# Kernel optimization log

Hardware: AMD Instinct MI355X
Metric: run time of the kernel (lower is better)

Reference implementation:

```python
import jax, jax.numpy as jnp
import numpy as np

NUM_SONGS = 2000
N1 = NUM_SONGS + 1  # incl. padding idx 0
EMB = 64
B = 32
S = 5    # num_prev_shows
M = 25   # max_songs_per_show


def setup_inputs() -> dict:
    key = jax.random.key(0)
    ks = jax.random.split(key, 32)
    def lin(k, i, o):
        kw, kb = jax.random.split(k)
        s = 1.0 / np.sqrt(i)
        return (jax.random.uniform(kw, (i, o), jnp.float32, -s, s),
                jax.random.uniform(kb, (o,), jnp.float32, -s, s))
    song_emb = jax.random.normal(ks[0], (N1, EMB), jnp.float32)
    song_emb = song_emb.at[0].set(0.0)  # padding_idx=0
    gcn_w1, gcn_b1 = lin(ks[1], EMB, EMB)
    gcn_w2, gcn_b2 = lin(ks[2], EMB, EMB)
    q_w, q_b = lin(ks[3], EMB, EMB)
    k_w, k_b = lin(ks[4], EMB, EMB)
    v_w, v_b = lin(ks[5], EMB, EMB)
    venue_t = jax.random.normal(ks[6], (200, EMB // 4), jnp.float32)
    tour_t = jax.random.normal(ks[7], (20, EMB // 4), jnp.float32)
    country_t = jax.random.normal(ks[8], (50, EMB // 8), jnp.float32)
    fest_t = jax.random.normal(ks[9], (2, EMB // 8), jnp.float32)
    mara_t = jax.random.normal(ks[10], (2, EMB // 8), jnp.float32)
    ctx_in = EMB // 2 + 3 * (EMB // 8)  # 56
    ctx_w, ctx_b = lin(ks[11], ctx_in, EMB)
    p1_w, p1_b = lin(ks[12], EMB * 3, EMB * 2)
    p2_w, p2_b = lin(ks[13], EMB * 2, EMB)
    p3_w, p3_b = lin(ks[14], EMB, 1)
    return {
        'song_ids': jax.random.randint(ks[20], (B,), 0, N1),
        'prev_setlists': jax.random.randint(ks[21], (B, S, M), 0, N1),
        'venue_ids': jax.random.randint(ks[22], (B,), 0, 200),
        'tour_ids': jax.random.randint(ks[23], (B,), 0, 20),
        'country_ids': jax.random.randint(ks[24], (B,), 0, 50),
        'is_festival': jax.random.randint(ks[25], (B,), 0, 2),
        'is_marathon': jax.random.randint(ks[26], (B,), 0, 2),
        'song_emb': song_emb,
        'gcn_w1': gcn_w1, 'gcn_b1': gcn_b1, 'gcn_w2': gcn_w2, 'gcn_b2': gcn_b2,
        'q_w': q_w, 'q_b': q_b, 'k_w': k_w, 'k_b': k_b, 'v_w': v_w, 'v_b': v_b,
        'venue_t': venue_t, 'tour_t': tour_t, 'country_t': country_t,
        'fest_t': fest_t, 'mara_t': mara_t,
        'ctx_w': ctx_w, 'ctx_b': ctx_b,
        'p1_w': p1_w, 'p1_b': p1_b, 'p2_w': p2_w, 'p2_b': p2_b,
        'p3_w': p3_w, 'p3_b': p3_b,
    }


def _build_adj(prev_setlists):
    # co-occurrence counts via one scatter-add (replaces nested python loops)
    b, s, m = prev_setlists.shape
    mask = prev_setlists > 0
    pair_ok = (mask[:, :, :, None] & mask[:, :, None, :]
               & ~jnp.eye(m, dtype=bool))  # exclude same position i==j
    flat_idx = (prev_setlists[:, :, :, None] * N1
                + prev_setlists[:, :, None, :]).reshape(b, -1)
    w = pair_ok.astype(jnp.float32).reshape(b, -1)
    adj = jnp.zeros((b, N1 * N1), jnp.float32)
    adj = adj.at[jnp.arange(b)[:, None], flat_idx].add(w)
    adj = adj.reshape(b, N1, N1)
    return adj / (adj.sum(axis=2, keepdims=True) + 1e-10)


def _forward(song_ids, prev_setlists, venue_ids, tour_ids, country_ids,
             is_festival, is_marathon, song_emb, gcn_w1, gcn_b1, gcn_w2,
             gcn_b2, q_w, q_b, k_w, k_b, v_w, v_b, venue_t, tour_t,
             country_t, fest_t, mara_t, ctx_w, ctx_b, p1_w, p1_b, p2_w,
             p2_b, p3_w, p3_b):
    b = song_ids.shape[0]
    adj = _build_adj(prev_setlists)                      # [B,N1,N1]
    x = jnp.broadcast_to(song_emb[None], (b, N1, EMB))   # [B,N1,E]
    for w_, b_ in ((gcn_w1, gcn_b1), (gcn_w2, gcn_b2)):
        agg = jnp.einsum('bnm,bme->bne', adj, x)
        x = jax.nn.relu(agg @ w_ + b_)
    song_embs = x
    # ragged masked-mean show embeddings
    mask = (prev_setlists > 0).astype(jnp.float32)       # [B,S,M]
    gathered = jax.vmap(lambda se, ids: se[ids])(song_embs, prev_setlists)  # [B,S,M,E]
    cnt = mask.sum(-1, keepdims=True)                    # [B,S,1]
    show_embs = jnp.where(cnt > 0,
                          (gathered * mask[..., None]).sum(2) / jnp.maximum(cnt, 1.0),
                          0.0)                           # [B,S,E]
    ctx = jnp.concatenate([venue_t[venue_ids], tour_t[tour_ids],
                           country_t[country_ids], fest_t[is_festival],
                           mara_t[is_marathon]], axis=-1)
    ctx = ctx @ ctx_w + ctx_b                            # [B,E]
    # temporal attention
    q = ctx @ q_w + q_b                                  # [B,E]
    k = show_embs @ k_w + k_b                            # [B,S,E]
    v = show_embs @ v_w + v_b
    scores = jnp.einsum('be,bse->bs', q, k) / jnp.sqrt(jnp.float32(EMB))
    attn = jax.nn.softmax(scores, axis=-1)
    attended = jnp.einsum('bs,bse->be', attn, v)
    cand = song_embs[jnp.arange(b), song_ids]
    h = jnp.concatenate([cand, ctx, attended], axis=-1)  # [B,3E]
    h = jax.nn.relu(h @ p1_w + p1_b)   # dropout is eval-mode identity
    h = jax.nn.relu(h @ p2_w + p2_b)
    logits = (h @ p3_w + p3_b).squeeze(-1)
    return jax.nn.sigmoid(logits)


def reference(song_ids, prev_setlists, venue_ids, tour_ids, country_ids,
              is_festival, is_marathon, song_emb, gcn_w1, gcn_b1, gcn_w2,
              gcn_b2, q_w, q_b, k_w, k_b, v_w, v_b, venue_t, tour_t,
              country_t, fest_t, mara_t, ctx_w, ctx_b, p1_w, p1_b, p2_w,
              p2_b, p3_w, p3_b):
    return _forward(song_ids, prev_setlists, venue_ids, tour_ids,
                    country_ids, is_festival, is_marathon, song_emb,
                    gcn_w1, gcn_b1, gcn_w2, gcn_b2, q_w, q_b, k_w, k_b,
                    v_w, v_b, venue_t, tour_t, country_t, fest_t, mara_t,
                    ctx_w, ctx_b, p1_w, p1_b, p2_w, p2_b, p3_w, p3_b)
```

## Files before the change

kernel.cpp:

```cpp
#include <hip/hip_runtime.h>
#include <hip/hip_bf16.h>

#define N1    2001
#define EMB   64
#define NSHOW 5
#define MSONG 25
#define NPOS  (NSHOW * MSONG)
#define MAXU  128
#define NT    1024

__global__ __launch_bounds__(NT, 4)
void setsgnn_kernel(
    const int* __restrict__ song_ids,
    const int* __restrict__ prev_setlists,
    const int* __restrict__ venue_ids,
    const int* __restrict__ tour_ids,
    const int* __restrict__ country_ids,
    const int* __restrict__ is_festival,
    const int* __restrict__ is_marathon,
    const float* __restrict__ song_emb,
    const float* __restrict__ gcn_w1, const float* __restrict__ gcn_b1,
    const float* __restrict__ gcn_w2, const float* __restrict__ gcn_b2,
    const float* __restrict__ q_w,  const float* __restrict__ q_b,
    const float* __restrict__ k_w,  const float* __restrict__ k_b,
    const float* __restrict__ v_w,  const float* __restrict__ v_b,
    const float* __restrict__ venue_t, const float* __restrict__ tour_t,
    const float* __restrict__ country_t, const float* __restrict__ fest_t,
    const float* __restrict__ mara_t,
    const float* __restrict__ ctx_w, const float* __restrict__ ctx_b,
    const float* __restrict__ p1_w,  const float* __restrict__ p1_b,
    const float* __restrict__ p2_w,  const float* __restrict__ p2_b,
    const float* __restrict__ p3_w,  const float* __restrict__ p3_b,
    float* __restrict__ out)
{
    const int b    = blockIdx.x;
    const int tid  = threadIdx.x;
    const int wv   = tid >> 6;
    const int lane = tid & 63;

    __shared__ __align__(16) float xb0[MAXU][EMB];
    __shared__ __align__(16) float xb1[MAXU][EMB];
    __shared__ __align__(16) float wlds[2][EMB][EMB];
    __shared__ __align__(16) float blds[2][EMB];
    __shared__ __align__(16) float bias_ctx[EMB], bias_q[EMB], bias_k[EMB], bias_v[EMB];
    __shared__ __align__(16) float bias_p1[128], bias_p2[EMB], bias_p3w[EMB];
    __shared__ float bias_p3b;
    __shared__ unsigned short idmap[N1];
    __shared__ int   sl[NPOS];
    __shared__ int   pmap[NPOS];
    __shared__ int   list_ids[MAXU];
    __shared__ float c_us[MAXU][NSHOW];
    __shared__ float occv[MAXU];
    __shared__ float invv[MAXU];
    __shared__ float cntm1[NSHOW];
    __shared__ int   cnt_show[NSHOW];
    __shared__ int   U_cnt;
    __shared__ float Xsum[NSHOW][EMB];
    __shared__ float XW[NSHOW][EMB];
    __shared__ float show_e[NSHOW][EMB];
    __shared__ float ctxin[56];
    __shared__ float ctxv[EMB];
    __shared__ float qv[EMB];
    __shared__ float kvatt[NSHOW][EMB];
    __shared__ float vatt[NSHOW][EMB];
    __shared__ float attnw[NSHOW];
    __shared__ float hbuf[3 * EMB];
    __shared__ float h1b[128];
    __shared__ float h2b[EMB];
    __shared__ float partial[1024];

    const float4 g0 = ((const float4*)gcn_w1)[tid];
    const float4 g1 = ((const float4*)gcn_w2)[tid];
    float4 bb;
    if (tid < 32) bb = (tid < 16) ? ((const float4*)gcn_b1)[tid]
                                  : ((const float4*)gcn_b2)[tid - 16];
    const int sid    = song_ids[b];
    const int vid    = venue_ids[b];
    const int tourid = tour_ids[b];
    const int cid    = country_ids[b];
    const int fid    = is_festival[b];
    const int mid    = is_marathon[b];

    for (int i = tid; i < N1; i += NT) idmap[i] = 0xFFFFu;
    if (tid < NPOS) sl[tid] = prev_setlists[b * NPOS + tid];
    if (tid == 0) U_cnt = 0;
    ((float4*)wlds)[tid]      = g0;
    ((float4*)wlds)[NT + tid] = g1;
    if (tid < 32) ((float4*)blds)[tid] = bb;
    {
        int r = tid - 256;
        if (r >= 0 && r < 16)        ((float4*)bias_ctx)[r]       = ((const float4*)ctx_b)[r];
        else if (r >= 16 && r < 32)  ((float4*)bias_q)[r - 16]    = ((const float4*)q_b)[r - 16];
        else if (r >= 32 && r < 48)  ((float4*)bias_k)[r - 32]    = ((const float4*)k_b)[r - 32];
        else if (r >= 48 && r < 64)  ((float4*)bias_v)[r - 48]    = ((const float4*)v_b)[r - 48];
        else if (r >= 64 && r < 96)  ((float4*)bias_p1)[r - 64]   = ((const float4*)p1_b)[r - 64];
        else if (r >= 96 && r < 112) ((float4*)bias_p2)[r - 96]   = ((const float4*)p2_b)[r - 96];
        else if (r >= 112 && r < 128)((float4*)bias_p3w)[r - 112] = ((const float4*)p3_w)[r - 112];
        else if (r == 128)           bias_p3b = p3_b[0];
    }
    __syncthreads();

    if (tid < NPOS) { int id = sl[tid]; if (id > 0) idmap[id] = 1u; }
    if (tid == 0) idmap[sid] = 1u;
    __syncthreads();

    for (int i = tid; i < N1; i += NT) {
        if (idmap[i] == 1u) {
            int u = atomicAdd(&U_cnt, 1);
            idmap[i] = (unsigned short)u;
            list_ids[u] = i;
        }
    }
    __syncthreads();
    const int U = U_cnt;

    if (tid < NPOS) { int id = sl[tid]; pmap[tid] = (id > 0) ? (int)idmap[id] : -1; }
    for (int t = tid; t < MAXU * NSHOW; t += NT) ((float*)c_us)[t] = 0.f;
    if (tid < NSHOW) {
        int c = 0;
        for (int i = 0; i < MSONG; i++) c += (sl[tid * MSONG + i] > 0) ? 1 : 0;
        cnt_show[tid] = c; cntm1[tid] = (float)(c - 1);
    }
    __syncthreads();

    if (tid < NPOS) { int pm = pmap[tid]; if (pm >= 0) atomicAdd(&c_us[pm][tid / MSONG], 1.f); }
    for (int t = tid; t < MAXU * (EMB / 4); t += NT) {
        int u = t >> 4, e4 = t & 15;
        float4 v = make_float4(0.f, 0.f, 0.f, 0.f);
        if (u < U) v = ((const float4*)(song_emb + list_ids[u] * EMB))[e4];
        *(float4*)&xb0[u][e4 * 4] = v;
    }
    __syncthreads();

    if (tid < MAXU) {
        float o = 0.f, r = 0.f;
        #pragma unroll
        for (int s = 0; s < NSHOW; s++) { float cc = c_us[tid][s]; o += cc; r += cc * cntm1[s]; }
        occv[tid] = o; invv[tid] = 1.f / (r + 1e-10f);
    }
    {
        int e = tid - MAXU;
        if (e >= 0 && e < 56) {
            float val;
            if (e < 16)      val = venue_t[vid * 16 + e];
            else if (e < 32) val = tour_t[tourid * 16 + (e - 16)];
            else if (e < 40) val = country_t[cid * 8 + (e - 32)];
            else if (e < 48) val = fest_t[fid * 8 + (e - 40)];
            else             val = mara_t[mid * 8 + (e - 48)];
            ctxin[e] = val;
        }
    }
    __syncthreads();

    if (tid < EMB) {
        float acc = bias_ctx[tid];
        #pragma unroll
        for (int e = 0; e < 56; e++) acc += ctxin[e] * ctx_w[e * EMB + tid];
        ctxv[tid] = acc;
    }
    __syncthreads();

    if (tid < EMB) {
        float acc = bias_q[tid];
        #pragma unroll
        for (int e = 0; e < EMB; e++) acc += ctxv[e] * q_w[e * EMB + tid];
        qv[tid] = acc;
    }
    if (tid >= EMB && tid < EMB + NSHOW * EMB) {
        int t = tid - EMB, s = t >> 6, e = t & 63;
        float acc = 0.f;
        #pragma unroll
        for (int i = 0; i < MSONG; i++) { int pm = pmap[s * MSONG + i]; if (pm >= 0) acc += xb0[pm][e]; }
        Xsum[s][e] = acc;
    }
    __syncthreads();

    {
        float wcol[EMB];
        for (int l = 0; l < 2; ++l) {
            float (*xc)[EMB] = l ? xb1 : xb0;
            float (*xn)[EMB] = l ? xb0 : xb1;

            #pragma unroll
            for (int e = 0; e < EMB; e++) wcol[e] = wlds[l][e][lane];
            if (tid < NSHOW * EMB) {
                int s = tid >> 6, col = tid & 63;
                float acc = 0.f;
                #pragma unroll
                for (int e = 0; e < EMB; e++) acc += Xsum[s][e] * wlds[l][e][col];
                XW[s][col] = acc;
            }
            const float bias = blds[l][lane];
            __syncthreads();

            float4 kreg, vreg;
            if (l == 1) { kreg = ((const float4*)k_w)[tid]; vreg = ((const float4*)v_w)[tid]; }

            for (int u = wv; u < U; u += 16) {
                float a0 = 0.f, a1 = 0.f, a2 = 0.f, a3 = 0.f;
                #pragma unroll
                for (int e4 = 0; e4 < 16; e4++) {
                    const float4 a = *(const float4*)&xc[u][e4 * 4];
                    a0 += a.x * wcol[e4 * 4];
                    a1 += a.y * wcol[e4 * 4 + 1];
                    a2 += a.z * wcol[e4 * 4 + 2];
                    a3 += a.w * wcol[e4 * 4 + 3];
                }
                float y   = (a0 + a1) + (a2 + a3);
                float acc = c_us[u][0] * XW[0][lane] + c_us[u][1] * XW[1][lane]
                          + c_us[u][2] * XW[2][lane] + c_us[u][3] * XW[3][lane]
                          + c_us[u][4] * XW[4][lane];
                float val = (acc - occv[u] * y) * invv[u] + bias;
                xn[u][lane] = fmaxf(val, 0.f);
            }
            if (l == 1) { ((float4*)wlds)[tid] = kreg; ((float4*)wlds)[NT + tid] = vreg; }
            __syncthreads();

            if (l == 0) {
                if (tid < NSHOW * EMB) {
                    int s = tid >> 6, e = tid & 63;
                    float acc = 0.f;
                    #pragma unroll
                    for (int i = 0; i < MSONG; i++) { int pm = pmap[s * MSONG + i]; if (pm >= 0) acc += xb1[pm][e]; }
                    Xsum[s][e] = acc;
                }
                __syncthreads();
            }
        }
    }

    const int kk1 = tid >> 7, o1 = tid & 127;
    const int kk2 = tid >> 6, o2 = lane;
    float p1wr[24], p2wr[8];
    #pragma unroll
    for (int j = 0; j < 24; j++) p1wr[j] = p1_w[(kk1 * 24 + j) * 128 + o1];
    #pragma unroll
    for (int j = 0; j < 8; j++)  p2wr[j] = p2_w[(kk2 * 8 + j) * 64 + o2];

    if (tid < NSHOW * EMB) {
        int s = tid >> 6, e = tid & 63;
        float acc = 0.f;
        #pragma unroll
        for (int i = 0; i < MSONG; i++) { int pm = pmap[s * MSONG + i]; if (pm >= 0) acc += xb0[pm][e]; }
        int cs = cnt_show[s];
        show_e[s][e] = (cs > 0) ? acc / (float)cs : 0.f;
    }
    __syncthreads();

    if (tid < 2 * NSHOW * EMB) {
        int m = (tid >= NSHOW * EMB) ? 1 : 0;
        int t = m ? tid - NSHOW * EMB : tid;
        int s = t >> 6, col = t & 63;
        float acc = m ? bias_v[col] : bias_k[col];
        #pragma unroll
        for (int e = 0; e < EMB; e++) acc += show_e[s][e] * wlds[m][e][col];
        if (m) vatt[s][col] = acc; else kvatt[s][col] = acc;
    }
    __syncthreads();

    if (wv < NSHOW) {
        float p = qv[lane] * kvatt[wv][lane];
        #pragma unroll
        for (int o = 32; o > 0; o >>= 1) p += __shfl_xor(p, o, 64);
        if (lane == 0) attnw[wv] = p * 0.125f;
    }
    __syncthreads();
    if (tid == 0) {
        float mx = attnw[0];
        for (int s = 1; s < NSHOW; s++) mx = fmaxf(mx, attnw[s]);
        float sum = 0.f;
        for (int s = 0; s < NSHOW; s++) { float ev = expf(attnw[s] - mx); attnw[s] = ev; sum += ev; }
        float isum = 1.f / sum;
        for (int s = 0; s < NSHOW; s++) attnw[s] *= isum;
    }
    __syncthreads();

    if (tid < EMB) {
        float acc = 0.f;
        #pragma unroll
        for (int s = 0; s < NSHOW; s++) acc += attnw[s] * vatt[s][tid];
        hbuf[2 * EMB + tid] = acc;
        hbuf[EMB + tid]     = ctxv[tid];
        hbuf[tid]           = xb0[(int)idmap[sid]][tid];
    }
    __syncthreads();

    {
        float acc = (kk1 == 0) ? bias_p1[o1] : 0.f;
        #pragma unroll
        for (int j = 0; j < 24; j++) acc += hbuf[kk1 * 24 + j] * p1wr[j];
        partial[kk1 * 128 + o1] = acc;
    }
    __syncthreads();
    if (tid < 128) {
        float acc = 0.f;
        #pragma unroll
        for (int kk = 0; kk < 8; kk++) acc += partial[kk * 128 + tid];
        h1b[tid] = fmaxf(acc, 0.f);
    }
    __syncthreads();

    {
        float acc = (kk2 == 0) ? bias_p2[o2] : 0.f;
        #pragma unroll
        for (int j = 0; j < 8; j++) acc += h1b[kk2 * 8 + j] * p2wr[j];
        partial[kk2 * 64 + o2] = acc;
    }
    __syncthreads();
    if (tid < 64) {
        float acc = 0.f;
        #pragma unroll
        for (int kk = 0; kk < 16; kk++) acc += partial[kk * 64 + tid];
        h2b[tid] = fmaxf(acc, 0.f);
    }
    __syncthreads();

    if (wv == 0) {
        float p = h2b[lane] * bias_p3w[lane];
        #pragma unroll
        for (int o = 32; o > 0; o >>= 1) p += __shfl_xor(p, o, 64);
        if (lane == 0) out[b] = 1.f / (1.f + expf(-(p + bias_p3b)));
    }
}

extern "C" void kernel_launch(void* const* d_in, const int* in_sizes, int n_in,
                              void* d_out, int out_size, void* d_ws, size_t ws_size,
                              hipStream_t stream) {
    (void)n_in; (void)out_size; (void)d_ws; (void)ws_size;
    const int B = in_sizes[0];
    setsgnn_kernel<<<B, NT, 0, stream>>>(
        (const int*)d_in[0], (const int*)d_in[1], (const int*)d_in[2],
        (const int*)d_in[3], (const int*)d_in[4], (const int*)d_in[5],
        (const int*)d_in[6],
        (const float*)d_in[7],
        (const float*)d_in[8],  (const float*)d_in[9],
        (const float*)d_in[10], (const float*)d_in[11],
        (const float*)d_in[12], (const float*)d_in[13],
        (const float*)d_in[14], (const float*)d_in[15],
        (const float*)d_in[16], (const float*)d_in[17],
        (const float*)d_in[18], (const float*)d_in[19],
        (const float*)d_in[20], (const float*)d_in[21],
        (const float*)d_in[22],
        (const float*)d_in[23], (const float*)d_in[24],
        (const float*)d_in[25], (const float*)d_in[26],
        (const float*)d_in[27], (const float*)d_in[28],
        (const float*)d_in[29], (const float*)d_in[30],
        (float*)d_out);
}
```

Baseline: 36.52 us.

## Restructure GCN layers: transposed padded weights, in-place register-tiled rows, ballot compaction

Stores the GCN and K/V weights transposed with padding in LDS so each lane reads its column contiguously. The GCN layer becomes a fixed 8-rows-per-wave register tile that updates xb0 in place, which drops the xb1 buffer and the per-lane weight-column copy. ctx_w and q_w are staged into LDS up front, the unique-id compaction uses a wave ballot with one atomic per wave, and several small setup phases are merged to remove barriers. In exchange it always computes all 128 padded rows, even when fewer unique songs exist, and it uses more LDS and registers per block.

```diff
diff --git a/kernel.cpp b/kernel.cpp
--- a/kernel.cpp
+++ b/kernel.cpp
@@ -1,5 +1,4 @@
 #include <hip/hip_runtime.h>
-#include <hip/hip_bf16.h>
 
 #define N1    2001
 #define EMB   64
@@ -8,8 +7,10 @@
 #define NPOS  (NSHOW * MSONG)
 #define MAXU  128
 #define NT    1024
-
-__global__ __launch_bounds__(NT, 4)
+#define WT    66
+
+__global__ __launch_bounds__(NT)
+__attribute__((amdgpu_waves_per_eu(4, 4)))
 void setsgnn_kernel(
     const int* __restrict__ song_ids,
     const int* __restrict__ prev_setlists,
@@ -39,8 +40,9 @@
     const int lane = tid & 63;
 
     __shared__ __align__(16) float xb0[MAXU][EMB];
-    __shared__ __align__(16) float xb1[MAXU][EMB];
-    __shared__ __align__(16) float wlds[2][EMB][EMB];
+    __shared__ __align__(16) float wldsT[2][EMB][WT];
+    __shared__ __align__(16) float ctxw_l[56][EMB];
+    __shared__ __align__(16) float qw_l[EMB][EMB];
     __shared__ __align__(16) float blds[2][EMB];
     __shared__ __align__(16) float bias_ctx[EMB], bias_q[EMB], bias_k[EMB], bias_v[EMB];
     __shared__ __align__(16) float bias_p1[128], bias_p2[EMB], bias_p3w[EMB];
@@ -69,11 +71,15 @@
     __shared__ float h2b[EMB];
     __shared__ float partial[1024];
 
-    const float4 g0 = ((const float4*)gcn_w1)[tid];
-    const float4 g1 = ((const float4*)gcn_w2)[tid];
+    const float4 g0  = ((const float4*)gcn_w1)[tid];
+    const float4 g1  = ((const float4*)gcn_w2)[tid];
+    const float4 qw4 = ((const float4*)q_w)[tid];
+    float4 cw4 = make_float4(0.f, 0.f, 0.f, 0.f);
+    if (tid < 896) cw4 = ((const float4*)ctx_w)[tid];
     float4 bb;
     if (tid < 32) bb = (tid < 16) ? ((const float4*)gcn_b1)[tid]
                                   : ((const float4*)gcn_b2)[tid - 16];
+    const int slr = (tid < NPOS) ? prev_setlists[b * NPOS + tid] : 0;
     const int sid    = song_ids[b];
     const int vid    = venue_ids[b];
     const int tourid = tour_ids[b];
@@ -82,10 +88,18 @@
     const int mid    = is_marathon[b];
 
     for (int i = tid; i < N1; i += NT) idmap[i] = 0xFFFFu;
-    if (tid < NPOS) sl[tid] = prev_setlists[b * NPOS + tid];
+    for (int t = tid; t < MAXU * NSHOW; t += NT) ((float*)c_us)[t] = 0.f;
+    if (tid < NPOS) sl[tid] = slr;
     if (tid == 0) U_cnt = 0;
-    ((float4*)wlds)[tid]      = g0;
-    ((float4*)wlds)[NT + tid] = g1;
+    {
+        const int e = tid >> 4, o0 = (tid * 4) & 63;
+        wldsT[0][o0    ][e] = g0.x; wldsT[0][o0 + 1][e] = g0.y;
+        wldsT[0][o0 + 2][e] = g0.z; wldsT[0][o0 + 3][e] = g0.w;
+        wldsT[1][o0    ][e] = g1.x; wldsT[1][o0 + 1][e] = g1.y;
+        wldsT[1][o0 + 2][e] = g1.z; wldsT[1][o0 + 3][e] = g1.w;
+    }
+    ((float4*)qw_l)[tid] = qw4;
+    if (tid < 896) ((float4*)ctxw_l)[tid] = cw4;
     if (tid < 32) ((float4*)blds)[tid] = bb;
     {
         int r = tid - 256;
@@ -105,8 +119,14 @@
     __syncthreads();
 
     for (int i = tid; i < N1; i += NT) {
-        if (idmap[i] == 1u) {
-            int u = atomicAdd(&U_cnt, 1);
+        const bool p = (idmap[i] == 1u);
+        const unsigned long long m = __ballot(p);
+        int base = 0;
+        if (lane == 0) { int c = __popcll(m); if (c) base = atomicAdd(&U_cnt, c); }
+        base = __shfl(base, 0, 64);
+        if (p) {
+            int r = __popcll(m & ((1ull << lane) - 1ull));
+            int u = base + r;
             idmap[i] = (unsigned short)u;
             list_ids[u] = i;
         }
@@ -114,16 +134,26 @@
     __syncthreads();
     const int U = U_cnt;
 
-    if (tid < NPOS) { int id = sl[tid]; pmap[tid] = (id > 0) ? (int)idmap[id] : -1; }
-    for (int t = tid; t < MAXU * NSHOW; t += NT) ((float*)c_us)[t] = 0.f;
-    if (tid < NSHOW) {
-        int c = 0;
-        for (int i = 0; i < MSONG; i++) c += (sl[tid * MSONG + i] > 0) ? 1 : 0;
-        cnt_show[tid] = c; cntm1[tid] = (float)(c - 1);
-    }
-    __syncthreads();
-
-    if (tid < NPOS) { int pm = pmap[tid]; if (pm >= 0) atomicAdd(&c_us[pm][tid / MSONG], 1.f); }
+    if (tid < NPOS) {
+        int id = sl[tid];
+        int pm = (id > 0) ? (int)idmap[id] : -1;
+        pmap[tid] = pm;
+        if (pm >= 0) atomicAdd(&c_us[pm][tid / MSONG], 1.f);
+    }
+    if (tid >= 128 && tid < 128 + NSHOW) {
+        int s = tid - 128, c = 0;
+        for (int i = 0; i < MSONG; i++) c += (sl[s * MSONG + i] > 0) ? 1 : 0;
+        cnt_show[s] = c; cntm1[s] = (float)(c - 1);
+    }
+    if (tid >= 144 && tid < 200) {
+        int e = tid - 144; float val;
+        if (e < 16)      val = venue_t[vid * 16 + e];
+        else if (e < 32) val = tour_t[tourid * 16 + (e - 16)];
+        else if (e < 40) val = country_t[cid * 8 + (e - 32)];
+        else if (e < 48) val = fest_t[fid * 8 + (e - 40)];
+        else             val = mara_t[mid * 8 + (e - 48)];
+        ctxin[e] = val;
+    }
     for (int t = tid; t < MAXU * (EMB / 4); t += NT) {
         int u = t >> 4, e4 = t & 15;
         float4 v = make_float4(0.f, 0.f, 0.f, 0.f);
@@ -138,97 +168,102 @@
         for (int s = 0; s < NSHOW; s++) { float cc = c_us[tid][s]; o += cc; r += cc * cntm1[s]; }
         occv[tid] = o; invv[tid] = 1.f / (r + 1e-10f);
     }
-    {
-        int e = tid - MAXU;
-        if (e >= 0 && e < 56) {
-            float val;
-            if (e < 16)      val = venue_t[vid * 16 + e];
-            else if (e < 32) val = tour_t[tourid * 16 + (e - 16)];
-            else if (e < 40) val = country_t[cid * 8 + (e - 32)];
-            else if (e < 48) val = fest_t[fid * 8 + (e - 40)];
-            else             val = mara_t[mid * 8 + (e - 48)];
-            ctxin[e] = val;
-        }
-    }
-    __syncthreads();
-
-    if (tid < EMB) {
-        float acc = bias_ctx[tid];
-        #pragma unroll
-        for (int e = 0; e < 56; e++) acc += ctxin[e] * ctx_w[e * EMB + tid];
-        ctxv[tid] = acc;
+    if (tid >= 128 && tid < 192) {
+        int col = tid - 128;
+        float acc = bias_ctx[col];
+        #pragma unroll
+        for (int e = 0; e < 56; e++) acc += ctxin[e] * ctxw_l[e][col];
+        ctxv[col] = acc;
+    }
+    if (wv >= 6 && wv < 11) {
+        int s = wv - 6;
+        int pm[MSONG];
+        #pragma unroll
+        for (int i = 0; i < MSONG; i++) pm[i] = pmap[s * MSONG + i];
+        float acc = 0.f;
+        #pragma unroll
+        for (int i = 0; i < MSONG; i++) if (pm[i] >= 0) acc += xb0[pm[i]][lane];
+        Xsum[s][lane] = acc;
     }
     __syncthreads();
 
     if (tid < EMB) {
         float acc = bias_q[tid];
         #pragma unroll
-        for (int e = 0; e < EMB; e++) acc += ctxv[e] * q_w[e * EMB + tid];
+        for (int e = 0; e < EMB; e++) acc += ctxv[e] * qw_l[e][tid];
         qv[tid] = acc;
     }
-    if (tid >= EMB && tid < EMB + NSHOW * EMB) {
-        int t = tid - EMB, s = t >> 6, e = t & 63;
-        float acc = 0.f;
-        #pragma unroll
-        for (int i = 0; i < MSONG; i++) { int pm = pmap[s * MSONG + i]; if (pm >= 0) acc += xb0[pm][e]; }
-        Xsum[s][e] = acc;
-    }
-    __syncthreads();
-
-    {
-        float wcol[EMB];
-        for (int l = 0; l < 2; ++l) {
-            float (*xc)[EMB] = l ? xb1 : xb0;
-            float (*xn)[EMB] = l ? xb0 : xb1;
-
-            #pragma unroll
-            for (int e = 0; e < EMB; e++) wcol[e] = wlds[l][e][lane];
-            if (tid < NSHOW * EMB) {
-                int s = tid >> 6, col = tid & 63;
-                float acc = 0.f;
-                #pragma unroll
-                for (int e = 0; e < EMB; e++) acc += Xsum[s][e] * wlds[l][e][col];
-                XW[s][col] = acc;
-            }
-            const float bias = blds[l][lane];
-            __syncthreads();
-
-            float4 kreg, vreg;
-            if (l == 1) { kreg = ((const float4*)k_w)[tid]; vreg = ((const float4*)v_w)[tid]; }
-
-            for (int u = wv; u < U; u += 16) {
-                float a0 = 0.f, a1 = 0.f, a2 = 0.f, a3 = 0.f;
-                #pragma unroll
-                for (int e4 = 0; e4 < 16; e4++) {
-                    const float4 a = *(const float4*)&xc[u][e4 * 4];
-                    a0 += a.x * wcol[e4 * 4];
-                    a1 += a.y * wcol[e4 * 4 + 1];
-                    a2 += a.z * wcol[e4 * 4 + 2];
-                    a3 += a.w * wcol[e4 * 4 + 3];
-                }
-                float y   = (a0 + a1) + (a2 + a3);
-                float acc = c_us[u][0] * XW[0][lane] + c_us[u][1] * XW[1][lane]
-                          + c_us[u][2] * XW[2][lane] + c_us[u][3] * XW[3][lane]
-                          + c_us[u][4] * XW[4][lane];
-                float val = (acc - occv[u] * y) * invv[u] + bias;
-                xn[u][lane] = fmaxf(val, 0.f);
-            }
-            if (l == 1) { ((float4*)wlds)[tid] = kreg; ((float4*)wlds)[NT + tid] = vreg; }
-            __syncthreads();
-
-            if (l == 0) {
-                if (tid < NSHOW * EMB) {
-                    int s = tid >> 6, e = tid & 63;
-                    float acc = 0.f;
-                    #pragma unroll
-                    for (int i = 0; i < MSONG; i++) { int pm = pmap[s * MSONG + i]; if (pm >= 0) acc += xb1[pm][e]; }
-                    Xsum[s][e] = acc;
-                }
-                __syncthreads();
-            }
+    if (tid >= 64 && tid < 64 + NSHOW * EMB) {
+        int t = tid - 64, s = t >> 6, col = t & 63;
+        float acc = 0.f;
+        #pragma unroll
+        for (int e = 0; e < EMB; e += 2) {
+            const float2 w2 = *(const float2*)&wldsT[0][col][e];
+            acc += Xsum[s][e] * w2.x + Xsum[s][e + 1] * w2.y;
         }
-    }
-
+        XW[s][col] = acc;
+    }
+    __syncthreads();
+
+    #define GCN_BODY(L)                                                          \
+    {                                                                            \
+        const float bias = blds[L][lane];                                        \
+        float y[8] = {0.f,0.f,0.f,0.f,0.f,0.f,0.f,0.f};                          \
+        _Pragma("unroll")                                                        \
+        for (int e4 = 0; e4 < 16; ++e4) {                                        \
+            float4 a[8];                                                         \
+            _Pragma("unroll")                                                    \
+            for (int uu = 0; uu < 8; ++uu)                                       \
+                a[uu] = *(const float4*)&xb0[(uu << 4) | wv][e4 * 4];            \
+            const float2 wa = *(const float2*)&wldsT[L][lane][e4 * 4];           \
+            const float2 wb = *(const float2*)&wldsT[L][lane][e4 * 4 + 2];       \
+            _Pragma("unroll")                                                    \
+            for (int uu = 0; uu < 8; ++uu)                                       \
+                y[uu] += a[uu].x * wa.x + a[uu].y * wa.y                         \
+                       + a[uu].z * wb.x + a[uu].w * wb.y;                        \
+        }                                                                        \
+        _Pragma("unroll")                                                        \
+        for (int uu = 0; uu < 8; ++uu) {                                         \
+            const int u = (uu << 4) | wv;                                        \
+            float acc = c_us[u][0] * XW[0][lane] + c_us[u][1] * XW[1][lane]      \
+                      + c_us[u][2] * XW[2][lane] + c_us[u][3] * XW[3][lane]      \
+                      + c_us[u][4] * XW[4][lane];                                \
+            float val = (acc - occv[u] * y[uu]) * invv[u] + bias;                \
+            xb0[u][lane] = fmaxf(val, 0.f);                                      \
+        }                                                                        \
+    }
+    GCN_BODY(0)
+    __syncthreads();
+
+    if (wv >= 6 && wv < 11) {
+        int s = wv - 6;
+        int pm[MSONG];
+        #pragma unroll
+        for (int i = 0; i < MSONG; i++) pm[i] = pmap[s * MSONG + i];
+        float acc = 0.f;
+        #pragma unroll
+        for (int i = 0; i < MSONG; i++) if (pm[i] >= 0) acc += xb0[pm[i]][lane];
+        Xsum[s][lane] = acc;
+    }
+    __syncthreads();
+
+    if (tid >= 64 && tid < 64 + NSHOW * EMB) {
+        int t = tid - 64, s = t >> 6, col = t & 63;
+        float acc = 0.f;
+        #pragma unroll
+        for (int e = 0; e < EMB; e += 2) {
+            const float2 w2 = *(const float2*)&wldsT[1][col][e];
+            acc += Xsum[s][e] * w2.x + Xsum[s][e + 1] * w2.y;
+        }
+        XW[s][col] = acc;
+    }
+    __syncthreads();
+
+    GCN_BODY(1)
+    __syncthreads();
+
+    const float4 kreg = ((const float4*)k_w)[tid];
+    const float4 vreg = ((const float4*)v_w)[tid];
     const int kk1 = tid >> 7, o1 = tid & 127;
     const int kk2 = tid >> 6, o2 = lane;
     float p1wr[24], p2wr[8];
@@ -237,13 +272,25 @@
     #pragma unroll
     for (int j = 0; j < 8; j++)  p2wr[j] = p2_w[(kk2 * 8 + j) * 64 + o2];
 
-    if (tid < NSHOW * EMB) {
-        int s = tid >> 6, e = tid & 63;
-        float acc = 0.f;
-        #pragma unroll
-        for (int i = 0; i < MSONG; i++) { int pm = pmap[s * MSONG + i]; if (pm >= 0) acc += xb0[pm][e]; }
+    if (wv >= 6 && wv < 11) {
+        int s = wv - 6;
+        int pm[MSONG];
+        #pragma unroll
+        for (int i = 0; i < MSONG; i++) pm[i] = pmap[s * MSONG + i];
+        float acc = 0.f;
+        #pragma unroll
+        for (int i = 0; i < MSONG; i++) if (pm[i] >= 0) acc += xb0[pm[i]][lane];
         int cs = cnt_show[s];
-        show_e[s][e] = (cs > 0) ? acc / (float)cs : 0.f;
+        show_e[s][lane] = (cs > 0) ? acc / (float)cs : 0.f;
+    }
+    if (tid < EMB)                      hbuf[tid] = xb0[(int)idmap[sid]][tid];
+    else if (tid >= 64 && tid < 128)    hbuf[EMB + (tid - 64)] = ctxv[tid - 64];
+    {
+        const int e = tid >> 4, o0 = (tid * 4) & 63;
+        wldsT[0][o0    ][e] = kreg.x; wldsT[0][o0 + 1][e] = kreg.y;
+        wldsT[0][o0 + 2][e] = kreg.z; wldsT[0][o0 + 3][e] = kreg.w;
+        wldsT[1][o0    ][e] = vreg.x; wldsT[1][o0 + 1][e] = vreg.y;
+        wldsT[1][o0 + 2][e] = vreg.z; wldsT[1][o0 + 3][e] = vreg.w;
     }
     __syncthreads();
 
@@ -253,7 +300,10 @@
         int s = t >> 6, col = t & 63;
         float acc = m ? bias_v[col] : bias_k[col];
         #pragma unroll
-        for (int e = 0; e < EMB; e++) acc += show_e[s][e] * wlds[m][e][col];
+        for (int e = 0; e < EMB; e += 2) {
+            const float2 w2 = *(const float2*)&wldsT[m][col][e];
+            acc += show_e[s][e] * w2.x + show_e[s][e + 1] * w2.y;
+        }
         if (m) vatt[s][col] = acc; else kvatt[s][col] = acc;
     }
     __syncthreads();
@@ -274,14 +324,11 @@
         for (int s = 0; s < NSHOW; s++) attnw[s] *= isum;
     }
     __syncthreads();
-
     if (tid < EMB) {
         float acc = 0.f;
         #pragma unroll
         for (int s = 0; s < NSHOW; s++) acc += attnw[s] * vatt[s][tid];
         hbuf[2 * EMB + tid] = acc;
-        hbuf[EMB + tid]     = ctxv[tid];
-        hbuf[tid]           = xb0[(int)idmap[sid]][tid];
     }
     __syncthreads();
 
```

After: 30.93 us. 15.3% less time.
